# Performance work log

Measured on AMD Instinct MI355X. Metric: run time of the kernel, lower is better.

The kernel has to match this reference:

```python
import jax, jax.numpy as jnp
import numpy as np

BATCH, T, N_STATE, N_IN, N_OUT = 256, 4096, 32, 8, 8
DT = 1e-3


def setup_inputs() -> dict:
    key = jax.random.key(0)
    k_u, k_x0, k_A, k_B, k_C, k_D = jax.random.split(key, 6)
    t = jnp.arange(T, dtype=jnp.float32) * DT
    u = jax.random.normal(k_u, (BATCH, T, N_IN), dtype=jnp.float32)
    x0 = jax.random.normal(k_x0, (BATCH, N_STATE), dtype=jnp.float32)
    # Stable-ish LTI system parameters
    A = (0.1 / np.sqrt(N_STATE)) * jax.random.normal(k_A, (N_STATE, N_STATE), dtype=jnp.float32) - 0.5 * jnp.eye(N_STATE, dtype=jnp.float32)
    B = jax.random.normal(k_B, (N_STATE, N_IN), dtype=jnp.float32) / np.sqrt(N_IN)
    C = jax.random.normal(k_C, (N_OUT, N_STATE), dtype=jnp.float32) / np.sqrt(N_STATE)
    D = jax.random.normal(k_D, (N_OUT, N_IN), dtype=jnp.float32) / np.sqrt(N_IN)
    return {"t": t, "u": u, "x0": x0, "A": A, "B": B, "C": C, "D": D}


def _dopri5_solve(t, u, x0, A, B):
    """Fixed-step Dopri5 (Dormand-Prince 5th order) on a uniform grid.

    Mirrors diffrax.diffeqsolve(Dopri5, ConstantStepSize, dt0=t[1], saveat=ts=t):
    one RK step per grid interval. u is evaluated at stage times via linear
    interpolation between grid samples.
    """
    dt = t[1] - t[0]

    def f(x, uu):  # vector field: dx = A x + B u
        return x @ A.T + uu @ B.T

    ut = jnp.swapaxes(u, 0, 1)  # [T, BATCH, N_IN]

    def step(x, uu):
        u0, u1 = uu
        du = u1 - u0
        k1 = f(x, u0)
        k2 = f(x + dt * (0.2 * k1), u0 + 0.2 * du)
        k3 = f(x + dt * (3.0 / 40.0 * k1 + 9.0 / 40.0 * k2), u0 + 0.3 * du)
        k4 = f(x + dt * (44.0 / 45.0 * k1 - 56.0 / 15.0 * k2 + 32.0 / 9.0 * k3), u0 + 0.8 * du)
        k5 = f(x + dt * (19372.0 / 6561.0 * k1 - 25360.0 / 2187.0 * k2 + 64448.0 / 6561.0 * k3 - 212.0 / 729.0 * k4), u0 + (8.0 / 9.0) * du)
        k6 = f(x + dt * (9017.0 / 3168.0 * k1 - 355.0 / 33.0 * k2 + 46732.0 / 5247.0 * k3 + 49.0 / 176.0 * k4 - 5103.0 / 18656.0 * k5), u1)
        xn = x + dt * (35.0 / 384.0 * k1 + 500.0 / 1113.0 * k3 + 125.0 / 192.0 * k4 - 2187.0 / 6784.0 * k5 + 11.0 / 84.0 * k6)
        return xn, xn

    _, xs_rest = jax.lax.scan(step, x0, (ut[:-1], ut[1:]))
    xs = jnp.concatenate([x0[None], xs_rest], axis=0)  # [T, BATCH, N_STATE]
    return jnp.swapaxes(xs, 0, 1)  # [BATCH, T, N_STATE]


def reference(t, u, x0, A, B, C, D):
    xs = _dopri5_solve(t, u, x0, A, B)          # state trajectory [BATCH, T, N_STATE]
    ys = xs @ C.T + u @ D.T                      # output y = C x + D u, [BATCH, T, N_OUT]
    return xs, ys
```

## Files before the change

kernel.cpp:

```cpp
#include <hip/hip_runtime.h>

#define BATCH 256
#define TT 4096
#define NS 32
#define NI 8
#define NO 8
#define LCH 64
#define NCHUNKS 64

#define WS_M  0
#define WS_N0 1024
#define WS_N1 1280
#define WS_ML 1536
#define WS_V  2560
#define WS_S  (2560 + BATCH * NCHUNKS * NS)

__device__ __forceinline__ float dot4(float4 a, float4 b) {
    return a.x * b.x + a.y * b.y + a.z * b.z + a.w * b.w;
}
__device__ __forceinline__ float4 ld4(const float* p) { return *(const float4*)p; }

__global__ __launch_bounds__(256) void k_pre(const float* __restrict__ tarr,
                                             const float* __restrict__ A,
                                             const float* __restrict__ B,
                                             float* __restrict__ ws) {
    __shared__ float sA[NS * NS], sB[NS * NI];
    __shared__ float Ka[6][NS * NS];
    __shared__ float Kb[6][NS * NI];
    __shared__ float Kc[6][NS * NI];
    __shared__ float Sa[NS * NS], Sb[NS * NI], Sc[NS * NI];
    __shared__ float Pq[2][NS * NS];

    const int tid = threadIdx.x;
    const float dt = tarr[1] - tarr[0];

    for (int e = tid; e < NS * NS; e += 256) sA[e] = A[e];
    for (int e = tid; e < NS * NI; e += 256) sB[e] = B[e];
    __syncthreads();
    for (int e = tid; e < NS * NS; e += 256) Ka[0][e] = sA[e];
    for (int e = tid; e < NS * NI; e += 256) { Kb[0][e] = sB[e]; Kc[0][e] = 0.f; }
    __syncthreads();

    const float atab[5][5] = {
        {0.2f, 0.f, 0.f, 0.f, 0.f},
        {3.f / 40.f, 9.f / 40.f, 0.f, 0.f, 0.f},
        {44.f / 45.f, -56.f / 15.f, 32.f / 9.f, 0.f, 0.f},
        {19372.f / 6561.f, -25360.f / 2187.f, 64448.f / 6561.f, -212.f / 729.f, 0.f},
        {9017.f / 3168.f, -355.f / 33.f, 46732.f / 5247.f, 49.f / 176.f, -5103.f / 18656.f}};
    const float ctab[6] = {0.f, 0.2f, 0.3f, 0.8f, 8.f / 9.f, 1.f};

    for (int st = 1; st <= 5; ++st) {
        for (int e = tid; e < NS * NS; e += 256) {
            float acc = 0.f;
            for (int j = 0; j < st; ++j) acc += atab[st - 1][j] * Ka[j][e];
            Sa[e] = acc;
        }
        for (int e = tid; e < NS * NI; e += 256) {
            float ab = 0.f, ac = 0.f;
            for (int j = 0; j < st; ++j) {
                ab += atab[st - 1][j] * Kb[j][e];
                ac += atab[st - 1][j] * Kc[j][e];
            }
            Sb[e] = ab; Sc[e] = ac;
        }
        __syncthreads();
        {
            const int j = tid & 31, ig = tid >> 5;
            for (int r = 0; r < 4; ++r) {
                const int row = ig + 8 * r;
                float acc = 0.f;
                for (int k = 0; k < NS; ++k) acc += sA[row * NS + k] * Sa[k * NS + j];
                Ka[st][row * NS + j] = sA[row * NS + j] + dt * acc;
            }
            const int jb = tid & 7, rb = tid >> 3;
            float ab = 0.f, ac = 0.f;
            for (int k = 0; k < NS; ++k) {
                ab += sA[rb * NS + k] * Sb[k * NI + jb];
                ac += sA[rb * NS + k] * Sc[k * NI + jb];
            }
            Kb[st][rb * NI + jb] = sB[rb * NI + jb] + dt * ab;
            Kc[st][rb * NI + jb] = ctab[st] * sB[rb * NI + jb] + dt * ac;
        }
        __syncthreads();
    }

    const float btab[6] = {35.f / 384.f, 0.f, 500.f / 1113.f, 125.f / 192.f,
                           -2187.f / 6784.f, 11.f / 84.f};
    for (int e = tid; e < NS * NS; e += 256) {
        float acc = 0.f;
        for (int i2 = 0; i2 < 6; ++i2) acc += btab[i2] * Ka[i2][e];
        const float m = dt * acc + (((e / NS) == (e % NS)) ? 1.f : 0.f);
        ws[WS_M + e] = m;
        Pq[0][e] = m;
    }
    for (int e = tid; e < NS * NI; e += 256) {
        float ap = 0.f, aq = 0.f;
        for (int i2 = 0; i2 < 6; ++i2) {
            ap += btab[i2] * Kb[i2][e];
            aq += btab[i2] * Kc[i2][e];
        }
        const float P = dt * ap, Q = dt * aq;
        ws[WS_N0 + e] = P - Q;
        ws[WS_N1 + e] = Q;
    }
    __syncthreads();

    int cur = 0;
    for (int itq = 0; itq < 6; ++itq) {
        const int j = tid & 31, ig = tid >> 5;
        for (int r = 0; r < 4; ++r) {
            const int row = ig + 8 * r;
            float acc = 0.f;
            for (int k = 0; k < NS; ++k) acc += Pq[cur][row * NS + k] * Pq[cur][k * NS + j];
            Pq[cur ^ 1][row * NS + j] = acc;
        }
        __syncthreads();
        cur ^= 1;
    }
    for (int e = tid; e < NS * NS; e += 256) ws[WS_ML + e] = Pq[cur][e];
}

template <bool P3>
__global__ __launch_bounds__(64, 1) void k_phase13(const float* __restrict__ u,
                                                   float* __restrict__ ws,
                                                   float* __restrict__ out,
                                                   const float* __restrict__ Cc,
                                                   const float* __restrict__ Dd) {
    const float* M = ws + WS_M;
    const float* N0 = ws + WS_N0;
    const float* N1 = ws + WS_N1;

    const int nch = P3 ? NCHUNKS : (NCHUNKS - 1);
    const int task = blockIdx.x;
    const int c = task % nch, g = task / nch;
    const int l = threadIdx.x;
    const int beta = l >> 3, s8 = l & 7;
    const int b = g * 8 + beta;

    float4 mq[4][8];
#pragma unroll
    for (int r = 0; r < 4; ++r)
#pragma unroll
        for (int jj = 0; jj < 8; ++jj) mq[r][jj] = ld4(M + (4 * s8 + r) * NS + 4 * jj);

    float4 n0q[4][2], n1q[4][2];
#pragma unroll
    for (int r = 0; r < 4; ++r) {
        n0q[r][0] = ld4(N0 + (4 * s8 + r) * NI);
        n0q[r][1] = ld4(N0 + (4 * s8 + r) * NI + 4);
        n1q[r][0] = ld4(N1 + (4 * s8 + r) * NI);
        n1q[r][1] = ld4(N1 + (4 * s8 + r) * NI + 4);
    }

    float4 cq[8], dq[2];
    if constexpr (P3) {
#pragma unroll
        for (int jj = 0; jj < 8; ++jj) cq[jj] = ld4(Cc + s8 * NS + 4 * jj);
        dq[0] = ld4(Dd + s8 * NI);
        dq[1] = ld4(Dd + s8 * NI + 4);
    }

    __shared__ float4 xb[2][8 * 9];

    const int t0 = c * LCH;
    const float* ub = u + (size_t)b * TT * NI;
    float4 u0a = ld4(ub + t0 * NI), u0b = ld4(ub + t0 * NI + 4);

    float4 mine;
    if constexpr (P3)
        mine = ld4(ws + WS_S + ((size_t)b * NCHUNKS + c) * NS + 4 * s8);
    else
        mine = make_float4(0.f, 0.f, 0.f, 0.f);

    xb[0][beta * 9 + s8] = mine;
    __syncthreads();

    float* yout = out + (size_t)BATCH * TT * NS;
    int cur = 0;
    for (int js = 0; js < LCH; ++js) {
        const int t = t0 + js;
        float4 xq[8];
#pragma unroll
        for (int jj = 0; jj < 8; ++jj) xq[jj] = xb[cur][beta * 9 + jj];

        if constexpr (P3) {
            *(float4*)(out + ((size_t)b * TT + t) * NS + 4 * s8) = mine;
            float yv = 0.f;
#pragma unroll
            for (int jj = 0; jj < 8; ++jj) yv += dot4(cq[jj], xq[jj]);
            yv += dot4(dq[0], u0a) + dot4(dq[1], u0b);
            yout[((size_t)b * TT + t) * NO + s8] = yv;
        }

        if (!P3 || js < LCH - 1) {
            const float4 u1a = ld4(ub + (t + 1) * NI);
            const float4 u1b = ld4(ub + (t + 1) * NI + 4);
            float w0 = dot4(n0q[0][0], u0a) + dot4(n0q[0][1], u0b) + dot4(n1q[0][0], u1a) + dot4(n1q[0][1], u1b);
            float w1 = dot4(n0q[1][0], u0a) + dot4(n0q[1][1], u0b) + dot4(n1q[1][0], u1a) + dot4(n1q[1][1], u1b);
            float w2 = dot4(n0q[2][0], u0a) + dot4(n0q[2][1], u0b) + dot4(n1q[2][0], u1a) + dot4(n1q[2][1], u1b);
            float w3 = dot4(n0q[3][0], u0a) + dot4(n0q[3][1], u0b) + dot4(n1q[3][0], u1a) + dot4(n1q[3][1], u1b);
#pragma unroll
            for (int jj = 0; jj < 8; ++jj) {
                const float4 xv = xq[jj];
                w0 += dot4(mq[0][jj], xv);
                w1 += dot4(mq[1][jj], xv);
                w2 += dot4(mq[2][jj], xv);
                w3 += dot4(mq[3][jj], xv);
            }
            mine = make_float4(w0, w1, w2, w3);
            xb[cur ^ 1][beta * 9 + s8] = mine;
            u0a = u1a;
            u0b = u1b;
        }
        __syncthreads();
        cur ^= 1;
    }

    if constexpr (!P3)
        *(float4*)(ws + WS_V + ((size_t)b * NCHUNKS + c) * NS + 4 * s8) = mine;
}

__global__ __launch_bounds__(64) void k_phase2(const float* __restrict__ x0,
                                               float* __restrict__ ws) {
    const float* ML = ws + WS_ML;
    const float* v = ws + WS_V;
    float* sst = ws + WS_S;
    const int b = blockIdx.x;
    const int l = threadIdx.x, i = l & 31, h = l >> 5;

    float mlr[16];
#pragma unroll
    for (int jj = 0; jj < 16; ++jj) mlr[jj] = ML[i * NS + 16 * h + jj];

    float x = x0[b * NS + i];
    for (int c = 0; c < NCHUNKS; ++c) {
        if (h == 0) sst[((size_t)b * NCHUNKS + c) * NS + i] = x;
        if (c == NCHUNKS - 1) break;
        float p = 0.f;
#pragma unroll
        for (int jj = 0; jj < 16; ++jj) p += mlr[jj] * __shfl(x, 16 * h + jj, 64);
        p += __shfl_xor(p, 32, 64);
        x = p + v[((size_t)b * NCHUNKS + c) * NS + i];
    }
}

extern "C" void kernel_launch(void* const* d_in, const int* in_sizes, int n_in,
                              void* d_out, int out_size, void* d_ws, size_t ws_size,
                              hipStream_t stream) {
    const float* t = (const float*)d_in[0];
    const float* u = (const float*)d_in[1];
    const float* x0 = (const float*)d_in[2];
    const float* A = (const float*)d_in[3];
    const float* B = (const float*)d_in[4];
    const float* C = (const float*)d_in[5];
    const float* D = (const float*)d_in[6];
    float* out = (float*)d_out;
    float* ws = (float*)d_ws;

    k_pre<<<dim3(1), dim3(256), 0, stream>>>(t, A, B, ws);
    k_phase13<false><<<dim3(32 * (NCHUNKS - 1)), dim3(64), 0, stream>>>(u, ws, out, C, D);
    k_phase2<<<dim3(BATCH), dim3(64), 0, stream>>>(x0, ws);
    k_phase13<true><<<dim3(32 * NCHUNKS), dim3(64), 0, stream>>>(u, ws, out, C, D);
}
```

Baseline: 415.9 us.

## Restructure chunked linear scan into hierarchical two-level scan with precomputed input kernels

Replaces the 64-chunk sequential phase-1 recurrence with a closed-form convolution: k_pre precomputes powers of the step matrix M and input-weight kernels W, so each chunk's forced response comes from one independent dot-product pass over 17 input samples. The chunk-carry scan becomes two levels (16 chunks within a super-chunk, then 16 super-chunks) to shorten the serial dependence chain. Phase 3 uses 16-step chunks, stages u and y through shared memory for coalesced loads and stores, and splits accumulators for ILP. The cost is more launches, more workspace traffic and a heavier single-block precompute.

```diff
diff --git a/kernel.cpp b/kernel.cpp
--- a/kernel.cpp
+++ b/kernel.cpp
@@ -5,40 +5,45 @@
 #define NS 32
 #define NI 8
 #define NO 8
-#define LCH 64
-#define NCHUNKS 64
-
-#define WS_M  0
-#define WS_N0 1024
-#define WS_N1 1280
-#define WS_ML 1536
-#define WS_V  2560
-#define WS_S  (2560 + BATCH * NCHUNKS * NS)
+#define LCH 16
+#define NCH 256
+#define NSUP 16
+#define SLEN 16
+
+#define WS_M    0
+#define WS_N0   1024
+#define WS_N1   1280
+#define WS_W    1536
+#define WS_PK   5888
+#define WS_MPOW 23296
+#define WS_V    40704
+#define WS_VV   (40704 + 2097152)
+#define WS_SS   (40704 + 2097152 + 131072)
 
 __device__ __forceinline__ float dot4(float4 a, float4 b) {
     return a.x * b.x + a.y * b.y + a.z * b.z + a.w * b.w;
 }
 __device__ __forceinline__ float4 ld4(const float* p) { return *(const float4*)p; }
 
-__global__ __launch_bounds__(256) void k_pre(const float* __restrict__ tarr,
-                                             const float* __restrict__ A,
-                                             const float* __restrict__ B,
-                                             float* __restrict__ ws) {
-    __shared__ float sA[NS * NS], sB[NS * NI];
-    __shared__ float Ka[6][NS * NS];
-    __shared__ float Kb[6][NS * NI];
-    __shared__ float Kc[6][NS * NI];
-    __shared__ float Sa[NS * NS], Sb[NS * NI], Sc[NS * NI];
-    __shared__ float Pq[2][NS * NS];
+__global__ __launch_bounds__(1024) void k_pre(const float* __restrict__ tarr,
+                                              const float* __restrict__ A,
+                                              const float* __restrict__ B,
+                                              float* __restrict__ ws) {
+    __shared__ float sA[1024], sB[256];
+    __shared__ float Ka[6][1024];
+    __shared__ float Kb[6][256], Kc[6][256];
+    __shared__ float Sa[1024], Sb[256], Sc[256];
+    __shared__ float Pq[2][1024];
 
     const int tid = threadIdx.x;
+    const int row = tid >> 5, col = tid & 31;
     const float dt = tarr[1] - tarr[0];
 
-    for (int e = tid; e < NS * NS; e += 256) sA[e] = A[e];
-    for (int e = tid; e < NS * NI; e += 256) sB[e] = B[e];
-    __syncthreads();
-    for (int e = tid; e < NS * NS; e += 256) Ka[0][e] = sA[e];
-    for (int e = tid; e < NS * NI; e += 256) { Kb[0][e] = sB[e]; Kc[0][e] = 0.f; }
+    sA[tid] = A[tid];
+    if (tid < 256) sB[tid] = B[tid];
+    __syncthreads();
+    Ka[0][tid] = sA[tid];
+    if (tid < 256) { Kb[0][tid] = sB[tid]; Kc[0][tid] = 0.f; }
     __syncthreads();
 
     const float atab[5][5] = {
@@ -50,99 +55,245 @@
     const float ctab[6] = {0.f, 0.2f, 0.3f, 0.8f, 8.f / 9.f, 1.f};
 
     for (int st = 1; st <= 5; ++st) {
-        for (int e = tid; e < NS * NS; e += 256) {
+        {
             float acc = 0.f;
-            for (int j = 0; j < st; ++j) acc += atab[st - 1][j] * Ka[j][e];
-            Sa[e] = acc;
-        }
-        for (int e = tid; e < NS * NI; e += 256) {
+            for (int j = 0; j < st; ++j) acc += atab[st - 1][j] * Ka[j][tid];
+            Sa[tid] = acc;
+        }
+        if (tid < 256) {
             float ab = 0.f, ac = 0.f;
             for (int j = 0; j < st; ++j) {
-                ab += atab[st - 1][j] * Kb[j][e];
-                ac += atab[st - 1][j] * Kc[j][e];
+                ab += atab[st - 1][j] * Kb[j][tid];
+                ac += atab[st - 1][j] * Kc[j][tid];
             }
-            Sb[e] = ab; Sc[e] = ac;
+            Sb[tid] = ab; Sc[tid] = ac;
         }
         __syncthreads();
         {
-            const int j = tid & 31, ig = tid >> 5;
-            for (int r = 0; r < 4; ++r) {
-                const int row = ig + 8 * r;
-                float acc = 0.f;
-                for (int k = 0; k < NS; ++k) acc += sA[row * NS + k] * Sa[k * NS + j];
-                Ka[st][row * NS + j] = sA[row * NS + j] + dt * acc;
-            }
-            const int jb = tid & 7, rb = tid >> 3;
+            float acc = 0.f;
+#pragma unroll
+            for (int k = 0; k < NS; ++k) acc += sA[row * NS + k] * Sa[k * NS + col];
+            Ka[st][tid] = sA[tid] + dt * acc;
+        }
+        if (tid < 256) {
+            const int rb = tid >> 3, jb = tid & 7;
             float ab = 0.f, ac = 0.f;
+#pragma unroll
             for (int k = 0; k < NS; ++k) {
                 ab += sA[rb * NS + k] * Sb[k * NI + jb];
                 ac += sA[rb * NS + k] * Sc[k * NI + jb];
             }
-            Kb[st][rb * NI + jb] = sB[rb * NI + jb] + dt * ab;
-            Kc[st][rb * NI + jb] = ctab[st] * sB[rb * NI + jb] + dt * ac;
+            Kb[st][tid] = sB[tid] + dt * ab;
+            Kc[st][tid] = ctab[st] * sB[tid] + dt * ac;
         }
         __syncthreads();
     }
 
     const float btab[6] = {35.f / 384.f, 0.f, 500.f / 1113.f, 125.f / 192.f,
                            -2187.f / 6784.f, 11.f / 84.f};
-    for (int e = tid; e < NS * NS; e += 256) {
+    float m;
+    {
         float acc = 0.f;
-        for (int i2 = 0; i2 < 6; ++i2) acc += btab[i2] * Ka[i2][e];
-        const float m = dt * acc + (((e / NS) == (e % NS)) ? 1.f : 0.f);
-        ws[WS_M + e] = m;
-        Pq[0][e] = m;
-    }
-    for (int e = tid; e < NS * NI; e += 256) {
+        for (int i2 = 0; i2 < 6; ++i2) acc += btab[i2] * Ka[i2][tid];
+        m = dt * acc + ((row == col) ? 1.f : 0.f);
+    }
+    ws[WS_M + tid] = m;
+    Pq[0][tid] = m;
+    Sa[tid] = m;
+    ws[WS_MPOW + tid] = (row == col) ? 1.f : 0.f;
+    ws[WS_MPOW + 1024 + tid] = m;
+    if (tid < 256) {
         float ap = 0.f, aq = 0.f;
         for (int i2 = 0; i2 < 6; ++i2) {
-            ap += btab[i2] * Kb[i2][e];
-            aq += btab[i2] * Kc[i2][e];
+            ap += btab[i2] * Kb[i2][tid];
+            aq += btab[i2] * Kc[i2][tid];
         }
         const float P = dt * ap, Q = dt * aq;
-        ws[WS_N0 + e] = P - Q;
-        ws[WS_N1 + e] = Q;
+        ws[WS_N0 + tid] = P - Q;
+        ws[WS_N1 + tid] = Q;
+        Sb[tid] = P - Q;
+        Sc[tid] = Q;
     }
     __syncthreads();
 
     int cur = 0;
-    for (int itq = 0; itq < 6; ++itq) {
-        const int j = tid & 31, ig = tid >> 5;
-        for (int r = 0; r < 4; ++r) {
-            const int row = ig + 8 * r;
-            float acc = 0.f;
-            for (int k = 0; k < NS; ++k) acc += Pq[cur][row * NS + k] * Pq[cur][k * NS + j];
-            Pq[cur ^ 1][row * NS + j] = acc;
-        }
+    for (int p = 2; p <= 16; ++p) {
+        float acc = 0.f;
+#pragma unroll
+        for (int k = 0; k < NS; ++k) acc += Pq[cur][row * NS + k] * Sa[k * NS + col];
+        Pq[cur ^ 1][tid] = acc;
         __syncthreads();
         cur ^= 1;
-    }
-    for (int e = tid; e < NS * NS; e += 256) ws[WS_ML + e] = Pq[cur][e];
-}
-
-template <bool P3>
-__global__ __launch_bounds__(64, 1) void k_phase13(const float* __restrict__ u,
-                                                   float* __restrict__ ws,
-                                                   float* __restrict__ out,
-                                                   const float* __restrict__ Cc,
-                                                   const float* __restrict__ Dd) {
+        ws[WS_MPOW + p * 1024 + tid] = acc;
+    }
+    Ka[0][tid] = Pq[cur][tid];
+    ws[WS_PK + tid] = (row == col) ? 1.f : 0.f;
+    ws[WS_PK + 1024 + tid] = Pq[cur][tid];
+    __syncthreads();
+    for (int k3 = 2; k3 <= 16; ++k3) {
+        float acc = 0.f;
+#pragma unroll
+        for (int k = 0; k < NS; ++k) acc += Pq[cur][row * NS + k] * Ka[0][k * NS + col];
+        Pq[cur ^ 1][tid] = acc;
+        __syncthreads();
+        cur ^= 1;
+        ws[WS_PK + k3 * 1024 + tid] = acc;
+    }
+    __syncthreads();
+
+    for (int idx = tid; idx < 17 * 256; idx += 1024) {
+        const int j = idx >> 8, e = idx & 255;
+        const int r = e >> 3, cc = e & 7;
+        float acc = 0.f;
+        if (j <= 15) {
+            const float* Mp = ws + WS_MPOW + (15 - j) * 1024 + r * NS;
+#pragma unroll
+            for (int k = 0; k < NS; ++k) acc += Mp[k] * Sb[k * NI + cc];
+        }
+        if (j >= 1) {
+            const float* Mp = ws + WS_MPOW + (16 - j) * 1024 + r * NS;
+#pragma unroll
+            for (int k = 0; k < NS; ++k) acc += Mp[k] * Sc[k * NI + cc];
+        }
+        ws[WS_W + idx] = acc;
+    }
+}
+
+__global__ __launch_bounds__(64) void k_v(const float* __restrict__ u,
+                                          float* __restrict__ ws) {
+    __shared__ __align__(16) float Wld[17 * 256];
+    const int l = threadIdx.x;
+    for (int i = l; i < 17 * 256; i += 64) Wld[i] = ws[WS_W + i];
+    __syncthreads();
+
+    const int b = blockIdx.x >> 2;
+    const int c = ((blockIdx.x & 3) << 6) + l;
+    if (c >= NCH - 1) return;
+
+    float acc[NS];
+#pragma unroll
+    for (int r = 0; r < NS; ++r) acc[r] = 0.f;
+
+    const float* ub = u + ((size_t)b * TT + (size_t)c * LCH) * NI;
+    for (int j = 0; j <= 16; ++j) {
+        const float4 ua = ld4(ub + j * NI);
+        const float4 ub4 = ld4(ub + j * NI + 4);
+        const float4* wj = (const float4*)(Wld + j * 256);
+#pragma unroll
+        for (int r = 0; r < NS; ++r)
+            acc[r] += dot4(wj[2 * r], ua) + dot4(wj[2 * r + 1], ub4);
+    }
+    float* vout = ws + WS_V + ((size_t)b * NCH + c) * NS;
+#pragma unroll
+    for (int r8 = 0; r8 < 8; ++r8)
+        *(float4*)(vout + 4 * r8) =
+            make_float4(acc[4 * r8], acc[4 * r8 + 1], acc[4 * r8 + 2], acc[4 * r8 + 3]);
+}
+
+__global__ __launch_bounds__(64) void k_scan2a(float* __restrict__ ws) {
+    const int b = blockIdx.x >> 4, S = blockIdx.x & 15;
+    const int l = threadIdx.x, i = l & 31, h = l >> 5;
+    const float* pk1 = ws + WS_PK + 1024;
+    float mlr[16];
+#pragma unroll
+    for (int jj = 0; jj < 16; ++jj) mlr[jj] = pk1[i * NS + 16 * h + jj];
+
+    float r = 0.f;
+    for (int k = 1; k <= 16; ++k) {
+        if (k == 16 && S == 15) break;
+        const int slot = (S << 4) + k - 1;
+        float p = 0.f;
+#pragma unroll
+        for (int jj = 0; jj < 16; ++jj) p += mlr[jj] * __shfl(r, 16 * h + jj, 64);
+        p += __shfl_xor(p, 32, 64);
+        float vv = 0.f;
+        if (h == 0) vv = ws[WS_V + ((size_t)b * NCH + slot) * NS + i];
+        r = p + vv;
+        if (h == 0) {
+            if (k < 16)
+                ws[WS_V + ((size_t)b * NCH + slot) * NS + i] = r;
+            else
+                ws[WS_VV + ((size_t)(b << 4) + S) * NS + i] = r;
+        }
+    }
+}
+
+__global__ __launch_bounds__(64) void k_scan2b(const float* __restrict__ x0,
+                                               float* __restrict__ ws) {
+    const int b = blockIdx.x;
+    const int l = threadIdx.x, i = l & 31, h = l >> 5;
+    const float* mlp = ws + WS_PK + 16 * 1024;
+    float mlr[16];
+#pragma unroll
+    for (int jj = 0; jj < 16; ++jj) mlr[jj] = mlp[i * NS + 16 * h + jj];
+
+    float x = x0[b * NS + i];
+    for (int S = 0; S < NSUP; ++S) {
+        if (h == 0) ws[WS_SS + ((size_t)(b << 4) + S) * NS + i] = x;
+        if (S == NSUP - 1) break;
+        float p = 0.f;
+#pragma unroll
+        for (int jj = 0; jj < 16; ++jj) p += mlr[jj] * __shfl(x, 16 * h + jj, 64);
+        p += __shfl_xor(p, 32, 64);
+        float vv = 0.f;
+        if (h == 0) vv = ws[WS_VV + ((size_t)(b << 4) + S) * NS + i];
+        x = p + vv;
+    }
+}
+
+__global__ __launch_bounds__(64) void k_phase3(const float* __restrict__ u,
+                                               float* __restrict__ ws,
+                                               float* __restrict__ out,
+                                               const float* __restrict__ Cc,
+                                               const float* __restrict__ Dd) {
+    const int c = blockIdx.x & 255;
+    const int g = blockIdx.x >> 8;
+    const int l = threadIdx.x, beta = l >> 3, s8 = l & 7;
+    const int b = g * 8 + beta;
+    const int S = c >> 4, k = c & 15;
+    const int t0 = c * LCH;
+
+    __shared__ float4 xb[2][8 * 9];
+    __shared__ __align__(16) float uld[8 * 136];
+    __shared__ __align__(16) float yld[8 * 136];
+
+    for (int f = l; f < 8 * 32; f += 64) {
+        const int task = f >> 5, e = f & 31;
+        const int bb = g * 8 + task;
+        const float4 val = *((const float4*)(u + ((size_t)bb * TT + t0) * NI) + e);
+        *((float4*)(uld + task * 136) + e) = val;
+    }
+
+    float4 mine;
+    {
+        const float* pk = ws + WS_PK + k * 1024;
+        const float* ss = ws + WS_SS + ((size_t)(b << 4) + S) * NS;
+        float4 sv[8];
+#pragma unroll
+        for (int jj = 0; jj < 8; ++jj) sv[jj] = ld4(ss + 4 * jj);
+        float a0 = 0.f, a1 = 0.f, a2 = 0.f, a3 = 0.f;
+#pragma unroll
+        for (int jj = 0; jj < 8; ++jj) {
+            a0 += dot4(ld4(pk + (4 * s8 + 0) * NS + 4 * jj), sv[jj]);
+            a1 += dot4(ld4(pk + (4 * s8 + 1) * NS + 4 * jj), sv[jj]);
+            a2 += dot4(ld4(pk + (4 * s8 + 2) * NS + 4 * jj), sv[jj]);
+            a3 += dot4(ld4(pk + (4 * s8 + 3) * NS + 4 * jj), sv[jj]);
+        }
+        if (k) {
+            const float4 rv = ld4(ws + WS_V + ((size_t)b * NCH + c - 1) * NS + 4 * s8);
+            a0 += rv.x; a1 += rv.y; a2 += rv.z; a3 += rv.w;
+        }
+        mine = make_float4(a0, a1, a2, a3);
+    }
+
     const float* M = ws + WS_M;
     const float* N0 = ws + WS_N0;
     const float* N1 = ws + WS_N1;
-
-    const int nch = P3 ? NCHUNKS : (NCHUNKS - 1);
-    const int task = blockIdx.x;
-    const int c = task % nch, g = task / nch;
-    const int l = threadIdx.x;
-    const int beta = l >> 3, s8 = l & 7;
-    const int b = g * 8 + beta;
-
     float4 mq[4][8];
 #pragma unroll
     for (int r = 0; r < 4; ++r)
 #pragma unroll
         for (int jj = 0; jj < 8; ++jj) mq[r][jj] = ld4(M + (4 * s8 + r) * NS + 4 * jj);
-
     float4 n0q[4][2], n1q[4][2];
 #pragma unroll
     for (int r = 0; r < 4; ++r) {
@@ -151,63 +302,52 @@
         n1q[r][0] = ld4(N1 + (4 * s8 + r) * NI);
         n1q[r][1] = ld4(N1 + (4 * s8 + r) * NI + 4);
     }
-
     float4 cq[8], dq[2];
-    if constexpr (P3) {
-#pragma unroll
-        for (int jj = 0; jj < 8; ++jj) cq[jj] = ld4(Cc + s8 * NS + 4 * jj);
-        dq[0] = ld4(Dd + s8 * NI);
-        dq[1] = ld4(Dd + s8 * NI + 4);
-    }
-
-    __shared__ float4 xb[2][8 * 9];
-
-    const int t0 = c * LCH;
-    const float* ub = u + (size_t)b * TT * NI;
-    float4 u0a = ld4(ub + t0 * NI), u0b = ld4(ub + t0 * NI + 4);
-
-    float4 mine;
-    if constexpr (P3)
-        mine = ld4(ws + WS_S + ((size_t)b * NCHUNKS + c) * NS + 4 * s8);
-    else
-        mine = make_float4(0.f, 0.f, 0.f, 0.f);
+#pragma unroll
+    for (int jj = 0; jj < 8; ++jj) cq[jj] = ld4(Cc + s8 * NS + 4 * jj);
+    dq[0] = ld4(Dd + s8 * NI);
+    dq[1] = ld4(Dd + s8 * NI + 4);
 
     xb[0][beta * 9 + s8] = mine;
     __syncthreads();
 
-    float* yout = out + (size_t)BATCH * TT * NS;
+    float4 u0a = *((const float4*)(uld + beta * 136));
+    float4 u0b = *((const float4*)(uld + beta * 136) + 1);
+
     int cur = 0;
+#pragma unroll 2
     for (int js = 0; js < LCH; ++js) {
         const int t = t0 + js;
         float4 xq[8];
 #pragma unroll
         for (int jj = 0; jj < 8; ++jj) xq[jj] = xb[cur][beta * 9 + jj];
 
-        if constexpr (P3) {
-            *(float4*)(out + ((size_t)b * TT + t) * NS + 4 * s8) = mine;
-            float yv = 0.f;
-#pragma unroll
-            for (int jj = 0; jj < 8; ++jj) yv += dot4(cq[jj], xq[jj]);
-            yv += dot4(dq[0], u0a) + dot4(dq[1], u0b);
-            yout[((size_t)b * TT + t) * NO + s8] = yv;
-        }
-
-        if (!P3 || js < LCH - 1) {
-            const float4 u1a = ld4(ub + (t + 1) * NI);
-            const float4 u1b = ld4(ub + (t + 1) * NI + 4);
-            float w0 = dot4(n0q[0][0], u0a) + dot4(n0q[0][1], u0b) + dot4(n1q[0][0], u1a) + dot4(n1q[0][1], u1b);
-            float w1 = dot4(n0q[1][0], u0a) + dot4(n0q[1][1], u0b) + dot4(n1q[1][0], u1a) + dot4(n1q[1][1], u1b);
-            float w2 = dot4(n0q[2][0], u0a) + dot4(n0q[2][1], u0b) + dot4(n1q[2][0], u1a) + dot4(n1q[2][1], u1b);
-            float w3 = dot4(n0q[3][0], u0a) + dot4(n0q[3][1], u0b) + dot4(n1q[3][0], u1a) + dot4(n1q[3][1], u1b);
-#pragma unroll
-            for (int jj = 0; jj < 8; ++jj) {
-                const float4 xv = xq[jj];
-                w0 += dot4(mq[0][jj], xv);
-                w1 += dot4(mq[1][jj], xv);
-                w2 += dot4(mq[2][jj], xv);
-                w3 += dot4(mq[3][jj], xv);
+        *(float4*)(out + ((size_t)b * TT + t) * NS + 4 * s8) = mine;
+        {
+            float ya = dot4(dq[0], u0a), yb = dot4(dq[1], u0b);
+#pragma unroll
+            for (int jj = 0; jj < 4; ++jj) {
+                ya += dot4(cq[jj], xq[jj]);
+                yb += dot4(cq[jj + 4], xq[jj + 4]);
             }
-            mine = make_float4(w0, w1, w2, w3);
+            yld[beta * 136 + js * NO + s8] = ya + yb;
+        }
+
+        if (js < LCH - 1) {
+            const float4 u1a = *((const float4*)(uld + beta * 136) + 2 * (js + 1));
+            const float4 u1b = *((const float4*)(uld + beta * 136) + 2 * (js + 1) + 1);
+            float wa[4], wb[4];
+#pragma unroll
+            for (int r = 0; r < 4; ++r) {
+                wa[r] = dot4(n0q[r][0], u0a) + dot4(n1q[r][0], u1a);
+                wb[r] = dot4(n0q[r][1], u0b) + dot4(n1q[r][1], u1b);
+#pragma unroll
+                for (int jj = 0; jj < 4; ++jj) {
+                    wa[r] += dot4(mq[r][jj], xq[jj]);
+                    wb[r] += dot4(mq[r][jj + 4], xq[jj + 4]);
+                }
+            }
+            mine = make_float4(wa[0] + wb[0], wa[1] + wb[1], wa[2] + wb[2], wa[3] + wb[3]);
             xb[cur ^ 1][beta * 9 + s8] = mine;
             u0a = u1a;
             u0b = u1b;
@@ -216,31 +356,12 @@
         cur ^= 1;
     }
 
-    if constexpr (!P3)
-        *(float4*)(ws + WS_V + ((size_t)b * NCHUNKS + c) * NS + 4 * s8) = mine;
-}
-
-__global__ __launch_bounds__(64) void k_phase2(const float* __restrict__ x0,
-                                               float* __restrict__ ws) {
-    const float* ML = ws + WS_ML;
-    const float* v = ws + WS_V;
-    float* sst = ws + WS_S;
-    const int b = blockIdx.x;
-    const int l = threadIdx.x, i = l & 31, h = l >> 5;
-
-    float mlr[16];
-#pragma unroll
-    for (int jj = 0; jj < 16; ++jj) mlr[jj] = ML[i * NS + 16 * h + jj];
-
-    float x = x0[b * NS + i];
-    for (int c = 0; c < NCHUNKS; ++c) {
-        if (h == 0) sst[((size_t)b * NCHUNKS + c) * NS + i] = x;
-        if (c == NCHUNKS - 1) break;
-        float p = 0.f;
-#pragma unroll
-        for (int jj = 0; jj < 16; ++jj) p += mlr[jj] * __shfl(x, 16 * h + jj, 64);
-        p += __shfl_xor(p, 32, 64);
-        x = p + v[((size_t)b * NCHUNKS + c) * NS + i];
+    float* yout = out + (size_t)BATCH * TT * NS;
+    float* ybase = yout + ((size_t)b * TT + t0) * NO;
+#pragma unroll
+    for (int q = 0; q < 4; ++q) {
+        const float4 val = *((const float4*)(yld + beta * 136) + (s8 * 4 + q));
+        *((float4*)ybase + s8 * 4 + q) = val;
     }
 }
 
@@ -257,8 +378,9 @@
     float* out = (float*)d_out;
     float* ws = (float*)d_ws;
 
-    k_pre<<<dim3(1), dim3(256), 0, stream>>>(t, A, B, ws);
-    k_phase13<false><<<dim3(32 * (NCHUNKS - 1)), dim3(64), 0, stream>>>(u, ws, out, C, D);
-    k_phase2<<<dim3(BATCH), dim3(64), 0, stream>>>(x0, ws);
-    k_phase13<true><<<dim3(32 * NCHUNKS), dim3(64), 0, stream>>>(u, ws, out, C, D);
-}
+    k_pre<<<dim3(1), dim3(1024), 0, stream>>>(t, A, B, ws);
+    k_v<<<dim3(BATCH * 4), dim3(64), 0, stream>>>(u, ws);
+    k_scan2a<<<dim3(BATCH * NSUP), dim3(64), 0, stream>>>(ws);
+    k_scan2b<<<dim3(BATCH), dim3(64), 0, stream>>>(x0, ws);
+    k_phase3<<<dim3(32 * NCH), dim3(64), 0, stream>>>(u, ws, out, C, D);
+}
```

Result: slower. 502.0 us (+20.7%).
